# Kernel optimization log

Hardware: AMD Instinct MI355X
Metric: run time of the kernel (lower is better)

Reference implementation:

```python
import jax, jax.numpy as jnp
import numpy as np

N, D, NH, NC, B, NL = 400, 256, 4, 2, 64, 2
HD = D // NH


def _ln(x, g, b, eps=1e-5):
    mu = x.mean(-1, keepdims=True)
    var = ((x - mu) ** 2).mean(-1, keepdims=True)
    return (x - mu) * jax.lax.rsqrt(var + eps) * g + b


def _mha(q, kv, wqkv, bqkv, wo, bo):
    # torch nn.MultiheadAttention (batch_first), eval mode
    wq, wk, wv = jnp.split(wqkv, 3, axis=0)
    bq, bk, bv = jnp.split(bqkv, 3, axis=0)
    Bsz, Sq, _ = q.shape
    Sk = kv.shape[1]
    qh = (q @ wq.T + bq).reshape(Bsz, Sq, NH, HD).transpose(0, 2, 1, 3)
    kh = (kv @ wk.T + bk).reshape(Bsz, Sk, NH, HD).transpose(0, 2, 1, 3)
    vh = (kv @ wv.T + bv).reshape(Bsz, Sk, NH, HD).transpose(0, 2, 1, 3)
    scores = jnp.einsum('bhqd,bhkd->bhqk', qh, kh) / jnp.sqrt(jnp.float32(HD))
    attn = jax.nn.softmax(scores, axis=-1)
    o = jnp.einsum('bhqk,bhkd->bhqd', attn, vh)
    o = o.transpose(0, 2, 1, 3).reshape(Bsz, Sq, D)
    return o @ wo.T + bo


def setup_inputs() -> dict:
    key = jax.random.key(0)
    ks = iter(jax.random.split(key, 64))
    w = lambda *s: (jax.random.normal(next(ks), s, dtype=jnp.float32) * 0.02)
    inp = {
        'fc_matrix': jax.random.uniform(next(ks), (B, N, N), dtype=jnp.float32),
        'sc_matrix': jax.random.uniform(next(ks), (B, N, N), dtype=jnp.float32),
        'proj_w': w(D, N), 'proj_b': jnp.zeros((D,), jnp.float32),
        'enc_qkv_w': w(NL, 3 * D, D), 'enc_qkv_b': jnp.zeros((NL, 3 * D), jnp.float32),
        'enc_out_w': w(NL, D, D), 'enc_out_b': jnp.zeros((NL, D), jnp.float32),
        'enc_lin1_w': w(NL, 4 * D, D), 'enc_lin1_b': jnp.zeros((NL, 4 * D), jnp.float32),
        'enc_lin2_w': w(NL, D, 4 * D), 'enc_lin2_b': jnp.zeros((NL, D), jnp.float32),
        'enc_n1_g': jnp.ones((NL, D), jnp.float32), 'enc_n1_b': jnp.zeros((NL, D), jnp.float32),
        'enc_n2_g': jnp.ones((NL, D), jnp.float32), 'enc_n2_b': jnp.zeros((NL, D), jnp.float32),
        'gcn_w1': w(D, N), 'gcn_b1': jnp.zeros((D,), jnp.float32),
        'gcn_w2': w(D, D), 'gcn_b2': jnp.zeros((D,), jnp.float32),
        'ca1_qkv_w': w(3 * D, D), 'ca1_qkv_b': jnp.zeros((3 * D,), jnp.float32),
        'ca1_out_w': w(D, D), 'ca1_out_b': jnp.zeros((D,), jnp.float32),
        'ca1_n_g': jnp.ones((D,), jnp.float32), 'ca1_n_b': jnp.zeros((D,), jnp.float32),
        'ca2_qkv_w': w(3 * D, D), 'ca2_qkv_b': jnp.zeros((3 * D,), jnp.float32),
        'ca2_out_w': w(D, D), 'ca2_out_b': jnp.zeros((D,), jnp.float32),
        'ca2_n_g': jnp.ones((D,), jnp.float32), 'ca2_n_b': jnp.zeros((D,), jnp.float32),
        'cls_w1': w(128, N * D), 'cls_b1': jnp.zeros((128,), jnp.float32),
        'cls_w2': w(NC, 128), 'cls_b2': jnp.zeros((NC,), jnp.float32),
    }
    return inp


def reference(fc_matrix, sc_matrix, proj_w, proj_b,
              enc_qkv_w, enc_qkv_b, enc_out_w, enc_out_b,
              enc_lin1_w, enc_lin1_b, enc_lin2_w, enc_lin2_b,
              enc_n1_g, enc_n1_b, enc_n2_g, enc_n2_b,
              gcn_w1, gcn_b1, gcn_w2, gcn_b2,
              ca1_qkv_w, ca1_qkv_b, ca1_out_w, ca1_out_b, ca1_n_g, ca1_n_b,
              ca2_qkv_w, ca2_qkv_b, ca2_out_w, ca2_out_b, ca2_n_g, ca2_n_b,
              cls_w1, cls_b1, cls_w2, cls_b2):
    # ---- FC branch: input proj + 2 post-norm transformer encoder layers ----
    h = fc_matrix @ proj_w.T + proj_b  # [B,N,D]
    for l in range(NL):
        a = _mha(h, h, enc_qkv_w[l], enc_qkv_b[l], enc_out_w[l], enc_out_b[l])
        h = _ln(h + a, enc_n1_g[l], enc_n1_b[l])
        ff = jax.nn.relu(h @ enc_lin1_w[l].T + enc_lin1_b[l]) @ enc_lin2_w[l].T + enc_lin2_b[l]
        h = _ln(h + ff, enc_n2_g[l], enc_n2_b[l])
    Z_F = h

    # ---- SC branch: dense-equivalent of per-sample nonzero()+GCNConv ----
    # all entries of sc are nonzero -> edge set == dense adjacency (self-loops present,
    # so add_remaining_self_loops is a no-op). deg = in-degree (column sums of weights).
    deg = sc_matrix.sum(axis=-2)  # [B,N]
    dinv = jnp.where(deg > 0, jax.lax.rsqrt(deg), 0.0)
    An = dinv[:, :, None] * sc_matrix * dinv[:, None, :]  # An[b,i,j] = dinv_i * w_ij * dinv_j
    h1 = jnp.einsum('bij,bid->bjd', An, sc_matrix @ gcn_w1.T) + gcn_b1  # aggregate src->dst
    h1 = jax.nn.relu(h1)
    Z_S = jnp.einsum('bij,bid->bjd', An, h1 @ gcn_w2.T) + gcn_b2  # [B,N,D]

    # ---- Cross attention (eval: dropout = identity) ----
    Z_F_cross = _ln(Z_F + _mha(Z_F, Z_S, ca1_qkv_w, ca1_qkv_b, ca1_out_w, ca1_out_b), ca1_n_g, ca1_n_b)
    Z_S_cross = _ln(Z_S + _mha(Z_S, Z_F, ca2_qkv_w, ca2_qkv_b, ca2_out_w, ca2_out_b), ca2_n_g, ca2_n_b)

    Z_joint = (Z_F_cross + Z_S_cross) * 0.5
    flat = Z_joint.reshape(Z_joint.shape[0], -1)  # [B, N*D]
    logits = jax.nn.relu(flat @ cls_w1.T + cls_b1) @ cls_w2.T + cls_b2
    return logits
```

## Files before the change

### kernel.cpp

```cpp
#include <hip/hip_runtime.h>
#include <math.h>

#define NB   64
#define NN   400
#define DD   256
#define NHH  4
#define HDD  64
#define MR   25600

typedef __attribute__((ext_vector_type(8))) short bf16x8;
typedef __attribute__((ext_vector_type(4))) float f32x4;

__device__ __forceinline__ short f2bf(float x) {
    union { float f; unsigned u; } v; v.f = x;
    return (short)((v.u + 0x7FFFu + ((v.u >> 16) & 1u)) >> 16);
}
__device__ __forceinline__ float bf2f(short s) {
    union { unsigned u; float f; } v; v.u = ((unsigned)(unsigned short)s) << 16;
    return v.f;
}
__device__ __forceinline__ void gl_lds16(const void* g, void* l) {
    __builtin_amdgcn_global_load_lds(
        (const __attribute__((address_space(1))) unsigned*)g,
        (__attribute__((address_space(3))) unsigned*)l, 16, 0, 0);
}
__device__ __forceinline__ void wait_vmcnt(int n) {
    switch (n) {
    case 0: asm volatile("s_waitcnt vmcnt(0)" ::: "memory"); break;
    case 1: asm volatile("s_waitcnt vmcnt(1)" ::: "memory"); break;
    case 2: asm volatile("s_waitcnt vmcnt(2)" ::: "memory"); break;
    case 3: asm volatile("s_waitcnt vmcnt(3)" ::: "memory"); break;
    case 4: asm volatile("s_waitcnt vmcnt(4)" ::: "memory"); break;
    default: asm volatile("s_waitcnt vmcnt(5)" ::: "memory"); break;
    }
}
__device__ __forceinline__ void barrier_raw() {
    __builtin_amdgcn_sched_barrier(0);
    __builtin_amdgcn_s_barrier();
    __builtin_amdgcn_sched_barrier(0);
}


__global__ __launch_bounds__(256) void gemm_p8(
    const short* __restrict__ A, int arows, long long sA,
    const short* __restrict__ B, int brows, long long sB,
    const float* __restrict__ bias,
    short* __restrict__ C, int crows, int crz, long long sCe,
    int M, int N, int Npad, int K, int relu)
{
    __shared__ short lds[24576];
    const int tid = threadIdx.x;
    const int z = blockIdx.z;
    const int m0 = blockIdx.x * 128, n0 = blockIdx.y * 128;
    const short* Ab = A + (size_t)z * sA;
    const short* Bb = B + (size_t)z * sB;

    const int w = tid >> 6, lane = tid & 63;
    const int quad = lane >> 4, l15 = lane & 15;
    const int wm = w & 1, wn = w >> 1;

    f32x4 acc[4][4] = {};

    const int KT = K >> 5;

    auto STAGE = [&](int buf, int kt) {
        const int gp0 = kt << 2;
        short* Al = lds + buf * 8192;
        short* Bl = Al + 4096;
#pragma unroll
        for (int i = 0; i < 4; ++i) {
            int c = i * 4 + w;
            int p = (c >> 1) & 3, hh = c & 1;
            if (c < 8)
                gl_lds16(Ab + ((size_t)(gp0 + p) * arows + m0 + hh * 64 + lane) * 8,
                         &Al[(p * 128 + hh * 64) * 8]);
            else
                gl_lds16(Bb + ((size_t)(gp0 + p) * brows + n0 + hh * 64 + lane) * 8,
                         &Bl[(p * 128 + hh * 64) * 8]);
        }
    };

    STAGE(0, 0);
    STAGE(1, 1);
    for (int kt = 0; kt < KT; ++kt) {
        wait_vmcnt(kt + 1 < KT ? 4 : 0);
        barrier_raw();
        if (kt + 2 < KT) STAGE((kt + 2) % 3, kt + 2);
        const short* Al = lds + (kt % 3) * 8192;
        const short* Bl = Al + 4096;
        bf16x8 af[4], bfr[4];
#pragma unroll
        for (int mi = 0; mi < 4; ++mi)
            af[mi] = *reinterpret_cast<const bf16x8*>(
                &Al[(quad * 128 + wm * 64 + mi * 16 + l15) * 8]);
#pragma unroll
        for (int ni = 0; ni < 4; ++ni)
            bfr[ni] = *reinterpret_cast<const bf16x8*>(
                &Bl[(quad * 128 + wn * 64 + ni * 16 + l15) * 8]);
#pragma unroll
        for (int mi = 0; mi < 4; ++mi)
#pragma unroll
            for (int ni = 0; ni < 4; ++ni)
                acc[mi][ni] = __builtin_amdgcn_mfma_f32_16x16x32_bf16(af[mi], bfr[ni], acc[mi][ni], 0, 0, 0);
    }
    __syncthreads();

#pragma unroll
    for (int mi = 0; mi < 4; ++mi) {
#pragma unroll
        for (int r = 0; r < 4; ++r) {
            int row = wm * 64 + mi * 16 + quad * 4 + r;
#pragma unroll
            for (int ni = 0; ni < 4; ++ni) {
                int col = wn * 64 + ni * 16 + l15;
                int gcol = n0 + col;
                float v = 0.0f;
                if (gcol < N) {
                    v = acc[mi][ni][r];
                    if (bias) v += bias[gcol];
                    if (relu) v = fmaxf(v, 0.0f);
                }
                lds[row * 136 + col] = f2bf(v);
            }
        }
    }
    __syncthreads();
    short* Cbz = C + (size_t)z * sCe;
    const long long zr = (long long)z * crz;
#pragma unroll
    for (int t = 0; t < 8; ++t) {
        int c = t * 256 + tid;
        int row = c & 127, p16 = c >> 7;
        int grow = m0 + row;
        int gcol0 = n0 + p16 * 8;
        if (grow < M && gcol0 < Npad) {
            bf16x8 v = *reinterpret_cast<const bf16x8*>(&lds[row * 136 + p16 * 8]);
            *reinterpret_cast<bf16x8*>(
                &Cbz[((size_t)(gcol0 >> 3) * crows + zr + grow) * 8]) = v;
        }
    }
}

__global__ __launch_bounds__(256) void gemm_ln(
    const short* __restrict__ A,
    const short* __restrict__ B, int brows,
    const float* __restrict__ bias,
    const short* __restrict__ resid,
    const float* __restrict__ g, const float* __restrict__ bb,
    short* __restrict__ out, int K)
{
    __shared__ short lds[30720];
    __shared__ float gs[256], bs[256], bi_s[256];
    __shared__ float red[2][4][64];
    const int tid = threadIdx.x;
    const int m0 = blockIdx.x * 64;
    const int w = tid >> 6, lane = tid & 63;
    const int quad = lane >> 4, l15 = lane & 15;
    gs[tid] = g[tid]; bs[tid] = bb[tid]; bi_s[tid] = bias[tid];

    f32x4 acc[4][4] = {};
    const int KT = K >> 5;

    auto STAGE = [&](int buf, int kt) {
        const int gp0 = kt << 2;
        short* Al = lds + buf * 10240;
        short* Bl = Al + 2048;
#pragma unroll
        for (int i = 0; i < 5; ++i) {
            int c = i * 4 + w;
            if (c < 4) {
                gl_lds16(A + ((size_t)(gp0 + c) * MR + m0 + lane) * 8, &Al[(c * 64) * 8]);
            } else {
                int cb = c - 4, p = cb >> 2, cq = cb & 3;
                gl_lds16(B + ((size_t)(gp0 + p) * brows + cq * 64 + lane) * 8,
                         &Bl[(p * 256 + cq * 64) * 8]);
            }
        }
    };

    STAGE(0, 0);
    STAGE(1, 1);
    for (int kt = 0; kt < KT; ++kt) {
        wait_vmcnt(kt + 1 < KT ? 5 : 0);
        barrier_raw();
        if (kt + 2 < KT) STAGE((kt + 2) % 3, kt + 2);
        const short* Al = lds + (kt % 3) * 10240;
        const short* Bl = Al + 2048;
        bf16x8 af[4], bfr[4];
#pragma unroll
        for (int mi = 0; mi < 4; ++mi)
            af[mi] = *reinterpret_cast<const bf16x8*>(
                &Al[(quad * 64 + mi * 16 + l15) * 8]);
#pragma unroll
        for (int ni = 0; ni < 4; ++ni)
            bfr[ni] = *reinterpret_cast<const bf16x8*>(
                &Bl[(quad * 256 + w * 64 + ni * 16 + l15) * 8]);
#pragma unroll
        for (int mi = 0; mi < 4; ++mi)
#pragma unroll
            for (int ni = 0; ni < 4; ++ni)
                acc[mi][ni] = __builtin_amdgcn_mfma_f32_16x16x32_bf16(af[mi], bfr[ni], acc[mi][ni], 0, 0, 0);
    }
    __syncthreads();

    short* rowt = lds;
#pragma unroll
    for (int mi = 0; mi < 4; ++mi)
#pragma unroll
        for (int ni = 0; ni < 4; ++ni) {
            int col = w * 64 + ni * 16 + l15;
#pragma unroll
            for (int r = 0; r < 4; ++r) {
                int row = mi * 16 + quad * 4 + r;
                rowt[row * 264 + w * 66 + ni * 16 + l15] = f2bf(acc[mi][ni][r] + bi_s[col]);
            }
        }
    __syncthreads();

    const int row = tid >> 2, part = tid & 3;
    const int grow = m0 + row;
    float vv[8][8];
    float sum = 0.0f, sq = 0.0f;
#pragma unroll
    for (int i = 0; i < 8; ++i) {
        int plane = part * 8 + i;
        bf16x8 rv = *reinterpret_cast<const bf16x8*>(resid + ((size_t)plane * MR + grow) * 8);
        bf16x8 tv = *reinterpret_cast<const bf16x8*>(&rowt[row * 264 + part * 66 + i * 8]);
#pragma unroll
        for (int e = 0; e < 8; ++e) {
            float v = bf2f(tv[e]) + bf2f(rv[e]);
            vv[i][e] = v; sum += v; sq += v * v;
        }
    }
    red[0][part][row] = sum; red[1][part][row] = sq;
    __syncthreads();
    sum = red[0][0][row] + red[0][1][row] + red[0][2][row] + red[0][3][row];
    sq  = red[1][0][row] + red[1][1][row] + red[1][2][row] + red[1][3][row];
    float mu = sum * (1.0f / 256.0f);
    float var = sq * (1.0f / 256.0f) - mu * mu;
    float rstd = 1.0f / sqrtf(fmaxf(var, 0.0f) + 1e-5f);
#pragma unroll
    for (int i = 0; i < 8; ++i) {
        int plane = part * 8 + i;
        bf16x8 o;
#pragma unroll
        for (int e = 0; e < 8; ++e)
            o[e] = f2bf((vv[i][e] - mu) * rstd * gs[plane * 8 + e] + bs[plane * 8 + e]);
        *reinterpret_cast<bf16x8*>(out + ((size_t)plane * MR + grow) * 8) = o;
    }
}

__global__ __launch_bounds__(256) void vtrans(
    const short* __restrict__ qkv, short* __restrict__ vT)
{
    __shared__ short tile[64][66];
    const int id = blockIdx.x;
    const int xcd = id & 7, rem = id >> 3;
    const int bh_hi = rem / 7, c = rem - bh_hi * 7;
    const int bh_i = bh_hi * 8 + xcd;
    const int h = bh_i & 3, b = bh_i >> 2;
    const int tid = threadIdx.x;
    const size_t bh = (size_t)bh_i;
    for (int t = tid; t < 512; t += 256) {
        int pp = t >> 6, l = t & 63;
        int j = c * 64 + l;
        bf16x8 v;
        if (j < NN)
            v = *reinterpret_cast<const bf16x8*>(
                qkv + (((size_t)(64 + 8 * h + pp)) * MR + (size_t)b * NN + j) * 8);
        else { for (int e = 0; e < 8; ++e) v[e] = 0; }
#pragma unroll
        for (int e = 0; e < 8; ++e) tile[l][pp * 8 + e] = v[e];
    }
    __syncthreads();
    for (int t = tid; t < 512; t += 256) {
        int kq = t >> 6, d = t & 63;
        int kp = c * 8 + kq;
        bf16x8 o;
#pragma unroll
        for (int e = 0; e < 8; ++e) o[e] = tile[kq * 8 + e][d];
        *reinterpret_cast<bf16x8*>(vT + ((bh * 56 + kp) * 64 + d) * 8) = o;
    }
}

__global__ __launch_bounds__(256, 3) void attn_p8(
    const short* __restrict__ qkv, const short* __restrict__ vT,
    short* __restrict__ Out)
{
    __shared__ short PS[26624];
    const int id = blockIdx.x;
    const int xcd = id & 7, rem = id >> 3;
    const int bh_hi = rem / 7, qt = rem - bh_hi * 7;
    const int bh_i = bh_hi * 8 + xcd;
    const int h = bh_i & 3, b = bh_i >> 2;
    const int tid = threadIdx.x;
    const int w = tid >> 6, lane = tid & 63;
    const int quad = lane >> 4, l15 = lane & 15;
    const size_t rowb = (size_t)b * NN;

    for (int j = w; j < 8; j += 4)
        gl_lds16(qkv + (((size_t)(8 * h + j)) * MR + rowb + qt * 64 + lane) * 8, &PS[j * 512]);
    __syncthreads();

    bf16x8 aq0 = *reinterpret_cast<const bf16x8*>(&PS[(quad * 64 + w * 16 + l15) * 8]);
    bf16x8 aq1 = *reinterpret_cast<const bf16x8*>(&PS[((4 + quad) * 64 + w * 16 + l15) * 8]);

    const short* Kb0 = qkv + ((size_t)(32 + 8 * h + quad) * MR + rowb + l15) * 8;
    const short* Kb1 = qkv + ((size_t)(36 + 8 * h + quad) * MR + rowb + l15) * 8;

    f32x4 sacc[25];
#pragma unroll
    for (int nt = 0; nt < 25; ++nt) { sacc[nt][0] = 0; sacc[nt][1] = 0; sacc[nt][2] = 0; sacc[nt][3] = 0; }
#pragma unroll
    for (int nt = 0; nt < 25; ++nt) {
        bf16x8 b0 = *reinterpret_cast<const bf16x8*>(Kb0 + nt * 128);
        bf16x8 b1 = *reinterpret_cast<const bf16x8*>(Kb1 + nt * 128);
        sacc[nt] = __builtin_amdgcn_mfma_f32_16x16x32_bf16(aq0, b0, sacc[nt], 0, 0, 0);
        sacc[nt] = __builtin_amdgcn_mfma_f32_16x16x32_bf16(aq1, b1, sacc[nt], 0, 0, 0);
    }

    float mx[4] = {-3e38f, -3e38f, -3e38f, -3e38f}, sm[4] = {0, 0, 0, 0};
#pragma unroll
    for (int nt = 0; nt < 25; ++nt)
#pragma unroll
        for (int r = 0; r < 4; ++r) mx[r] = fmaxf(mx[r], sacc[nt][r]);
#pragma unroll
    for (int r = 0; r < 4; ++r) {
        mx[r] = fmaxf(mx[r], __shfl_xor(mx[r], 1));
        mx[r] = fmaxf(mx[r], __shfl_xor(mx[r], 2));
        mx[r] = fmaxf(mx[r], __shfl_xor(mx[r], 4));
        mx[r] = fmaxf(mx[r], __shfl_xor(mx[r], 8));
    }
#pragma unroll
    for (int nt = 0; nt < 25; ++nt)
#pragma unroll
        for (int r = 0; r < 4; ++r) {
            float e = __expf((sacc[nt][r] - mx[r]) * 0.125f);
            sacc[nt][r] = e;
            sm[r] += e;
        }
#pragma unroll
    for (int r = 0; r < 4; ++r) {
        sm[r] += __shfl_xor(sm[r], 1);
        sm[r] += __shfl_xor(sm[r], 2);
        sm[r] += __shfl_xor(sm[r], 4);
        sm[r] += __shfl_xor(sm[r], 8);
    }
    __syncthreads();

#pragma unroll
    for (int nt = 0; nt < 25; ++nt)
#pragma unroll
        for (int r = 0; r < 4; ++r) {
            int colk = nt * 16 + l15;
            PS[((colk >> 3) * 64 + w * 16 + quad * 4 + r) * 8 + (colk & 7)] = f2bf(sacc[nt][r]);
        }
    for (int idx = tid; idx < 1024; idx += 256) PS[25600 + idx] = 0;

    f32x4 oacc[4];
#pragma unroll
    for (int dt = 0; dt < 4; ++dt) { oacc[dt][0] = 0; oacc[dt][1] = 0; oacc[dt][2] = 0; oacc[dt][3] = 0; }
    __syncthreads();

    const short* Vb = vT + (((size_t)bh_i * 56 + quad) * 64 + l15) * 8;
#pragma unroll
    for (int kt = 0; kt < 13; ++kt) {
        bf16x8 pa = *reinterpret_cast<const bf16x8*>(
            &PS[((kt * 4 + quad) * 64 + w * 16 + l15) * 8]);
#pragma unroll
        for (int dt = 0; dt < 4; ++dt) {
            bf16x8 vb = *reinterpret_cast<const bf16x8*>(Vb + kt * 2048 + dt * 128);
            oacc[dt] = __builtin_amdgcn_mfma_f32_16x16x32_bf16(pa, vb, oacc[dt], 0, 0, 0);
        }
    }
#pragma unroll
    for (int r = 0; r < 4; ++r) {
        int row = qt * 64 + w * 16 + quad * 4 + r;
        if (row >= NN) continue;
        float inv = 1.0f / sm[r];
#pragma unroll
        for (int dt = 0; dt < 4; ++dt) {
            int col = dt * 16 + l15;
            Out[(((size_t)(8 * h + (col >> 3))) * MR + rowb + row) * 8 + (col & 7)] =
                f2bf(oacc[dt][r] * inv);
        }
    }
}

__global__ void conv_p8(const float* __restrict__ src, short* __restrict__ dst,
                        int R, int K, int Kp, int PR)
{
    const int G = Kp >> 3;
    int idx = blockIdx.x * 256 + threadIdx.x;
    if (idx >= R * G) return;
    int r = idx / G, g = idx - r * G;
    int k0 = g << 3;
    bf16x8 o;
    if (k0 + 8 <= K) {
        const float4 v0 = *reinterpret_cast<const float4*>(src + (size_t)r * K + k0);
        const float4 v1 = *reinterpret_cast<const float4*>(src + (size_t)r * K + k0 + 4);
        o[0] = f2bf(v0.x); o[1] = f2bf(v0.y); o[2] = f2bf(v0.z); o[3] = f2bf(v0.w);
        o[4] = f2bf(v1.x); o[5] = f2bf(v1.y); o[6] = f2bf(v1.z); o[7] = f2bf(v1.w);
    } else {
#pragma unroll
        for (int e = 0; e < 8; ++e) {
            int k = k0 + e;
            o[e] = (k < K) ? f2bf(src[(size_t)r * K + k]) : (short)0;
        }
    }
    *reinterpret_cast<bf16x8*>(dst + ((size_t)g * PR + r) * 8) = o;
}

__global__ __launch_bounds__(256) void w1_p8(
    const float* __restrict__ W1, short* __restrict__ Wp)
{
    __shared__ float tile[128][129];
    const int k0 = blockIdx.x * 128;
    const int tid = threadIdx.x;
    for (int t = 0; t < 16; ++t) {
        int idx = t * 256 + tid;
        int r = idx >> 5, k4 = idx & 31;
        float4 v = *(const float4*)(W1 + (size_t)r * 102400 + k0 + k4 * 4);
        tile[r][k4 * 4 + 0] = v.x; tile[r][k4 * 4 + 1] = v.y;
        tile[r][k4 * 4 + 2] = v.z; tile[r][k4 * 4 + 3] = v.w;
    }
    __syncthreads();
    for (int t = 0; t < 8; ++t) {
        int idx = t * 256 + tid;
        int pidx = idx >> 7, r = idx & 127;
        bf16x8 o;
#pragma unroll
        for (int e = 0; e < 8; ++e) o[e] = f2bf(tile[r][pidx * 8 + e]);
        *reinterpret_cast<bf16x8*>(Wp + (((size_t)(k0 >> 3) + pidx) * 128 + r) * 8) = o;
    }
}

__global__ void colsum_dinv(const float* __restrict__ sc, float* __restrict__ dinv)
{
    int b = blockIdx.y;
    int j = blockIdx.x * 256 + threadIdx.x;
    if (j >= NN) return;
    const float* p = sc + (size_t)b * NN * NN + j;
    float s = 0.0f;
    for (int i = 0; i < NN; ++i) s += p[(size_t)i * NN];
    dinv[b * NN + j] = (s > 0.0f) ? 1.0f / sqrtf(s) : 0.0f;
}

__global__ __launch_bounds__(256) void sc_prep(
    const float* __restrict__ sc, const float* __restrict__ dinv,
    short* __restrict__ scb, short* __restrict__ anT)
{
    __shared__ float tile[64][65];
    const int b = blockIdx.z;
    const int i0 = blockIdx.y * 64, j0 = blockIdx.x * 64;
    const int tid = threadIdx.x;
    const float* sb = sc + (size_t)b * NN * NN;
    short* scbb = scb + (size_t)b * 56 * 512 * 8;
    short* anTb = anT + (size_t)b * 56 * 512 * 8;
    for (int e = tid; e < 4096; e += 256) {
        int r = e >> 6, c = e & 63;
        int i = i0 + r, j = j0 + c;
        tile[r][c] = (i < NN && j < NN) ? sb[(size_t)i * NN + j] : 0.0f;
    }
    __syncthreads();
    for (int e = tid; e < 4096; e += 256) {
        int r = e >> 6, c = e & 63;
        int i = i0 + r, j = j0 + c;
        scbb[((size_t)(j >> 3) * 512 + i) * 8 + (j & 7)] = f2bf(tile[r][c]);
        float v = 0.0f;
        if (i < NN && j < NN) v = tile[r][c] * dinv[b * NN + i] * dinv[b * NN + j];
        anTb[((size_t)(i >> 3) * 512 + j) * 8 + (i & 7)] = f2bf(v);
    }
}

__global__ __launch_bounds__(256) void cls_gemm(
    const short* __restrict__ C1, const short* __restrict__ C2,
    const short* __restrict__ Wp, float* __restrict__ partial)
{
    __shared__ short Al[32 * 64 * 8];
    __shared__ short Wl[8 * 128 * 8];
    const int j = blockIdx.x;
    const int tid = threadIdx.x;
    const int w = tid >> 6, lane = tid & 63;
    const int quad = lane >> 4, l15 = lane & 15;

    for (int s = 0; s < 8; ++s) {
        int idx = s * 256 + tid;
        int p = idx >> 6, b = idx & 63;
        size_t ad = ((size_t)p * MR + (size_t)b * NN + j) * 8;
        bf16x8 a = *reinterpret_cast<const bf16x8*>(C1 + ad);
        bf16x8 c = *reinterpret_cast<const bf16x8*>(C2 + ad);
        bf16x8 o;
#pragma unroll
        for (int e = 0; e < 8; ++e) o[e] = f2bf(0.5f * (bf2f(a[e]) + bf2f(c[e])));
        *reinterpret_cast<bf16x8*>(&Al[(p * 64 + b) * 8]) = o;
    }

    f32x4 acc[4][2] = {};
    const size_t wp0 = (size_t)j * 32;
    for (int s = 0; s < 4; ++s) {
#pragma unroll
        for (int pp = 0; pp < 2; ++pp) {
            int p = w + pp * 4;
            gl_lds16(Wp + ((wp0 + s * 8 + p) * 128 + lane) * 8,      &Wl[(p * 128) * 8]);
            gl_lds16(Wp + ((wp0 + s * 8 + p) * 128 + 64 + lane) * 8, &Wl[(p * 128 + 64) * 8]);
        }
        __syncthreads();
#pragma unroll
        for (int kb = 0; kb < 2; ++kb) {
            bf16x8 af[4], bfr[2];
#pragma unroll
            for (int mi = 0; mi < 4; ++mi)
                af[mi] = *reinterpret_cast<const bf16x8*>(
                    &Al[((s * 8 + kb * 4 + quad) * 64 + mi * 16 + l15) * 8]);
#pragma unroll
            for (int ni = 0; ni < 2; ++ni)
                bfr[ni] = *reinterpret_cast<const bf16x8*>(
                    &Wl[((kb * 4 + quad) * 128 + w * 32 + ni * 16 + l15) * 8]);
#pragma unroll
            for (int mi = 0; mi < 4; ++mi)
#pragma unroll
                for (int ni = 0; ni < 2; ++ni)
                    acc[mi][ni] = __builtin_amdgcn_mfma_f32_16x16x32_bf16(af[mi], bfr[ni], acc[mi][ni], 0, 0, 0);
        }
        __syncthreads();
    }
    float* pj = partial + (size_t)j * 8192;
#pragma unroll
    for (int mi = 0; mi < 4; ++mi)
#pragma unroll
        for (int r = 0; r < 4; ++r) {
            int row = mi * 16 + quad * 4 + r;
#pragma unroll
            for (int ni = 0; ni < 2; ++ni)
                pj[row * 128 + w * 32 + ni * 16 + l15] = acc[mi][ni][r];
        }
}

__global__ void cls_reduce(const float* __restrict__ partial, float* __restrict__ clsh)
{
    int o = blockIdx.x * 256 + threadIdx.x;
    float s = 0.0f;
    for (int kb = 0; kb < 400; ++kb) s += partial[(size_t)kb * 8192 + o];
    clsh[o] = s;
}

__global__ void logits_final(
    const float* __restrict__ clsh, const float* __restrict__ b1,
    const float* __restrict__ w2, const float* __restrict__ b2,
    float* __restrict__ out)
{
    __shared__ float t[128];
    int b = blockIdx.x;
    int tid = threadIdx.x;
    t[tid] = fmaxf(clsh[b * 128 + tid] + b1[tid], 0.0f);
    __syncthreads();
    if (tid < 2) {
        float s = b2[tid];
        for (int o = 0; o < 128; ++o) s += t[o] * w2[tid * 128 + o];
        out[b * 2 + tid] = s;
    }
}

extern "C" void kernel_launch(void* const* d_in, const int* in_sizes, int n_in,
                              void* d_out, int out_size, void* d_ws, size_t ws_size,
                              hipStream_t stream)
{
    const float* fc        = (const float*)d_in[0];
    const float* sc        = (const float*)d_in[1];
    const float* proj_w    = (const float*)d_in[2];
    const float* proj_b    = (const float*)d_in[3];
    const float* enc_qkv_w = (const float*)d_in[4];
    const float* enc_qkv_b = (const float*)d_in[5];
    const float* enc_out_w = (const float*)d_in[6];
    const float* enc_out_b = (const float*)d_in[7];
    const float* enc_l1_w  = (const float*)d_in[8];
    const float* enc_l1_b  = (const float*)d_in[9];
    const float* enc_l2_w  = (const float*)d_in[10];
    const float* enc_l2_b  = (const float*)d_in[11];
    const float* enc_n1_g  = (const float*)d_in[12];
    const float* enc_n1_b  = (const float*)d_in[13];
    const float* enc_n2_g  = (const float*)d_in[14];
    const float* enc_n2_b  = (const float*)d_in[15];
    const float* gcn_w1    = (const float*)d_in[16];
    const float* gcn_b1    = (const float*)d_in[17];
    const float* gcn_w2    = (const float*)d_in[18];
    const float* gcn_b2    = (const float*)d_in[19];
    const float* ca1_qkv_w = (const float*)d_in[20];
    const float* ca1_qkv_b = (const float*)d_in[21];
    const float* ca1_out_w = (const float*)d_in[22];
    const float* ca1_out_b = (const float*)d_in[23];
    const float* ca1_n_g   = (const float*)d_in[24];
    const float* ca1_n_b   = (const float*)d_in[25];
    const float* ca2_qkv_w = (const float*)d_in[26];
    const float* ca2_qkv_b = (const float*)d_in[27];
    const float* ca2_out_w = (const float*)d_in[28];
    const float* ca2_out_b = (const float*)d_in[29];
    const float* ca2_n_g   = (const float*)d_in[30];
    const float* ca2_n_b   = (const float*)d_in[31];
    const float* cls_w1    = (const float*)d_in[32];
    const float* cls_b1    = (const float*)d_in[33];
    const float* cls_w2    = (const float*)d_in[34];
    const float* cls_b2    = (const float*)d_in[35];

    char* wsb = (char*)d_ws;
    size_t off = 0;
    auto alloc = [&](size_t bytes) { char* r = wsb + off; off += (bytes + 255) & ~(size_t)255; return r; };
    short* bufBig = (short*)alloc((size_t)MR * 1024 * 2);
    short* fcb    = (short*)alloc((size_t)56 * MR * 8 * 2);
    short* anT    = (short*)alloc((size_t)NB * 56 * 512 * 8 * 2);
    short* bufH   = (short*)alloc((size_t)32 * MR * 8 * 2);
    short* bufA   = (short*)alloc((size_t)32 * MR * 8 * 2);
    short* bufC   = (short*)alloc((size_t)32 * MR * 8 * 2);
    short* bufZS  = (short*)alloc((size_t)32 * MR * 8 * 2);
    short* vT     = (short*)alloc((size_t)NB * NHH * 56 * 64 * 8 * 2);
    short* w1b    = (short*)alloc((size_t)12800 * 128 * 8 * 2);
    short* projwb = (short*)alloc((size_t)56 * 256 * 8 * 2);
    short* qkvwb  = (short*)alloc((size_t)32 * 1536 * 8 * 2);
    short* outwb  = (short*)alloc((size_t)32 * 512 * 8 * 2);
    short* l1wb   = (short*)alloc((size_t)32 * 2048 * 8 * 2);
    short* l2wb   = (short*)alloc((size_t)128 * 512 * 8 * 2);
    short* gw1b   = (short*)alloc((size_t)56 * 256 * 8 * 2);
    short* gw2b   = (short*)alloc((size_t)32 * 256 * 8 * 2);
    short* c1qb   = (short*)alloc((size_t)32 * 768 * 8 * 2);
    short* c1ob   = (short*)alloc((size_t)32 * 256 * 8 * 2);
    short* c2qb   = (short*)alloc((size_t)32 * 768 * 8 * 2);
    short* c2ob   = (short*)alloc((size_t)32 * 256 * 8 * 2);
    float* dinv   = (float*)alloc((size_t)MR * 4);
    float* clsh   = (float*)alloc((size_t)NB * 128 * 4);
    short* scb = bufBig;
    short* XT1 = bufBig + (size_t)64 * 56 * 512 * 8;
    short* h1  = bufBig;
    short* XT2 = XT1;
    float* partial = (float*)fcb;

    dim3 blk(256);
    auto cgrid = [](long long n) { return dim3((unsigned)((n + 255) / 256)); };

    conv_p8<<<cgrid((long long)MR * 56), blk, 0, stream>>>(fc, fcb, MR, 400, 448, MR);
    conv_p8<<<cgrid(256 * 56), blk, 0, stream>>>(proj_w, projwb, 256, 400, 448, 256);
    conv_p8<<<cgrid(1536 * 32), blk, 0, stream>>>(enc_qkv_w, qkvwb, 1536, 256, 256, 1536);
    conv_p8<<<cgrid(512 * 32), blk, 0, stream>>>(enc_out_w, outwb, 512, 256, 256, 512);
    conv_p8<<<cgrid(2048 * 32), blk, 0, stream>>>(enc_l1_w, l1wb, 2048, 256, 256, 2048);
    conv_p8<<<cgrid(512 * 128), blk, 0, stream>>>(enc_l2_w, l2wb, 512, 1024, 1024, 512);
    conv_p8<<<cgrid(256 * 56), blk, 0, stream>>>(gcn_w1, gw1b, 256, 400, 448, 256);
    conv_p8<<<cgrid(256 * 32), blk, 0, stream>>>(gcn_w2, gw2b, 256, 256, 256, 256);
    conv_p8<<<cgrid(768 * 32), blk, 0, stream>>>(ca1_qkv_w, c1qb, 768, 256, 256, 768);
    conv_p8<<<cgrid(256 * 32), blk, 0, stream>>>(ca1_out_w, c1ob, 256, 256, 256, 256);
    conv_p8<<<cgrid(768 * 32), blk, 0, stream>>>(ca2_qkv_w, c2qb, 768, 256, 256, 768);
    conv_p8<<<cgrid(256 * 32), blk, 0, stream>>>(ca2_out_w, c2ob, 256, 256, 256, 256);
    w1_p8<<<800, blk, 0, stream>>>(cls_w1, w1b);

    gemm_p8<<<dim3(200, 2, 1), blk, 0, stream>>>(
        fcb, MR, 0, projwb, 256, 0, proj_b, bufH, MR, 0, 0, MR, 256, 256, 448, 0);
    for (int l = 0; l < 2; ++l) {
        gemm_p8<<<dim3(200, 6, 1), blk, 0, stream>>>(
            bufH, MR, 0, qkvwb + (size_t)l * 768 * 8, 1536, 0, enc_qkv_b + l * 768,
            bufBig, MR, 0, 0, MR, 768, 768, 256, 0);
        vtrans<<<dim3(1792), blk, 0, stream>>>(bufBig, vT);
        attn_p8<<<dim3(1792), blk, 0, stream>>>(bufBig, vT, bufA);
        gemm_ln<<<400, blk, 0, stream>>>(
            bufA, outwb + (size_t)l * 256 * 8, 512, enc_out_b + l * 256,
            bufH, enc_n1_g + l * DD, enc_n1_b + l * DD, bufH, 256);
        gemm_p8<<<dim3(200, 8, 1), blk, 0, stream>>>(
            bufH, MR, 0, l1wb + (size_t)l * 1024 * 8, 2048, 0, enc_l1_b + l * 1024,
            bufBig, MR, 0, 0, MR, 1024, 1024, 256, 1);
        gemm_ln<<<400, blk, 0, stream>>>(
            bufBig, l2wb + (size_t)l * 256 * 8, 512, enc_l2_b + l * 256,
            bufH, enc_n2_g + l * DD, enc_n2_b + l * DD, bufH, 1024);
    }

    colsum_dinv<<<dim3(2, NB), blk, 0, stream>>>(sc, dinv);
    sc_prep<<<dim3(7, 7, NB), blk, 0, stream>>>(sc, dinv, scb, anT);
    gemm_p8<<<dim3(2, 4, NB), blk, 0, stream>>>(
        gw1b, 256, 0, scb, 512, 56LL * 512 * 8, nullptr,
        XT1, 256, 0, 56LL * 256 * 8, 256, 400, 448, 448, 0);
    gemm_p8<<<dim3(4, 2, NB), blk, 0, stream>>>(
        anT, 512, 56LL * 512 * 8, XT1, 256, 56LL * 256 * 8, gcn_b1,
        h1, 512, 0, 32LL * 512 * 8, 400, 256, 256, 448, 1);
    gemm_p8<<<dim3(2, 4, NB), blk, 0, stream>>>(
        gw2b, 256, 0, h1, 512, 32LL * 512 * 8, nullptr,
        XT2, 256, 0, 56LL * 256 * 8, 256, 400, 448, 256, 0);
    gemm_p8<<<dim3(4, 2, NB), blk, 0, stream>>>(
        anT, 512, 56LL * 512 * 8, XT2, 256, 56LL * 256 * 8, gcn_b2,
        bufZS, MR, 400, 0, 400, 256, 256, 448, 0);

    gemm_p8<<<dim3(200, 2, 1), blk, 0, stream>>>(
        bufH, MR, 0, c1qb, 768, 0, ca1_qkv_b, bufBig, MR, 0, 0, MR, 256, 256, 256, 0);
    gemm_p8<<<dim3(200, 4, 1), blk, 0, stream>>>(
        bufZS, MR, 0, c1qb + 256 * 8, 768, 0, ca1_qkv_b + 256,
        bufBig + (size_t)32 * MR * 8, MR, 0, 0, MR, 512, 512, 256, 0);
    vtrans<<<dim3(1792), blk, 0, stream>>>(bufBig, vT);
    attn_p8<<<dim3(1792), blk, 0, stream>>>(bufBig, vT, bufA);
    gemm_ln<<<400, blk, 0, stream>>>(
        bufA, c1ob, 256, ca1_out_b, bufH, ca1_n_g, ca1_n_b, bufC, 256);

    gemm_p8<<<dim3(200, 2, 1), blk, 0, stream>>>(
        bufZS, MR, 0, c2qb, 768, 0, ca2_qkv_b, bufBig, MR, 0, 0, MR, 256, 256, 256, 0);
    gemm_p8<<<dim3(200, 4, 1), blk, 0, stream>>>(
        bufH, MR, 0, c2qb + 256 * 8, 768, 0, ca2_qkv_b + 256,
        bufBig + (size_t)32 * MR * 8, MR, 0, 0, MR, 512, 512, 256, 0);
    vtrans<<<dim3(1792), blk, 0, stream>>>(bufBig, vT);
    attn_p8<<<dim3(1792), blk, 0, stream>>>(bufBig, vT, bufA);
    gemm_ln<<<400, blk, 0, stream>>>(
        bufA, c2ob, 256, ca2_out_b, bufZS, ca2_n_g, ca2_n_b, bufZS, 256);

    cls_gemm<<<400, blk, 0, stream>>>(bufC, bufZS, w1b, partial);
    cls_reduce<<<32, blk, 0, stream>>>(partial, clsh);
    logits_final<<<NB, 128, 0, stream>>>(clsh, cls_b1, cls_w2, cls_b2, (float*)d_out);
}
```

Measured before the change: 970.3 us.

## Enlarge GEMM tile to 256x128 with 512 threads and batch weight conversions

The bf16 MFMA GEMM now computes a 256x128 output tile per block using 8 waves, up from 128x128 with 4. Each B tile loaded into LDS is therefore reused across twice as many rows, which cuts global traffic for the weight operand. The LDS ring buffer, stage mapping, vmcnt wait count and epilogue indexing are resized to match, and all launch grids are halved along M. Separately, eleven weight float-to-bf16 conversion launches are merged into one segmented kernel to save launch overhead. The `__launch_bounds__(512, 4)` hint may cap registers tightly enough to force accumulator spills, and fewer blocks means less parallelism on the smaller GCN GEMMs.

```diff
diff --git a/kernel.cpp b/kernel.cpp
--- a/kernel.cpp
+++ b/kernel.cpp
@@ -41,23 +41,23 @@
 }
 
 
-__global__ __launch_bounds__(256) void gemm_p8(
+__global__ __launch_bounds__(512, 4) void gemm_p8(
     const short* __restrict__ A, int arows, long long sA,
     const short* __restrict__ B, int brows, long long sB,
     const float* __restrict__ bias,
     short* __restrict__ C, int crows, int crz, long long sCe,
     int M, int N, int Npad, int K, int relu)
 {
-    __shared__ short lds[24576];
+    __shared__ short lds[36864];
     const int tid = threadIdx.x;
     const int z = blockIdx.z;
-    const int m0 = blockIdx.x * 128, n0 = blockIdx.y * 128;
+    const int m0 = blockIdx.x * 256, n0 = blockIdx.y * 128;
     const short* Ab = A + (size_t)z * sA;
     const short* Bb = B + (size_t)z * sB;
 
     const int w = tid >> 6, lane = tid & 63;
     const int quad = lane >> 4, l15 = lane & 15;
-    const int wm = w & 1, wn = w >> 1;
+    const int wm = w & 3, wn = w >> 2;
 
     f32x4 acc[4][4] = {};
 
@@ -65,34 +65,36 @@
 
     auto STAGE = [&](int buf, int kt) {
         const int gp0 = kt << 2;
-        short* Al = lds + buf * 8192;
-        short* Bl = Al + 4096;
-#pragma unroll
-        for (int i = 0; i < 4; ++i) {
-            int c = i * 4 + w;
-            int p = (c >> 1) & 3, hh = c & 1;
-            if (c < 8)
+        short* Al = lds + buf * 12288;
+        short* Bl = Al + 8192;
+#pragma unroll
+        for (int i = 0; i < 3; ++i) {
+            int c = i * 8 + w;
+            if (c < 16) {
+                int p = c >> 2, hh = c & 3;
                 gl_lds16(Ab + ((size_t)(gp0 + p) * arows + m0 + hh * 64 + lane) * 8,
-                         &Al[(p * 128 + hh * 64) * 8]);
-            else
+                         &Al[(p * 256 + hh * 64) * 8]);
+            } else {
+                int cb = c - 16, p = cb >> 1, hh = cb & 1;
                 gl_lds16(Bb + ((size_t)(gp0 + p) * brows + n0 + hh * 64 + lane) * 8,
                          &Bl[(p * 128 + hh * 64) * 8]);
+            }
         }
     };
 
     STAGE(0, 0);
     STAGE(1, 1);
     for (int kt = 0; kt < KT; ++kt) {
-        wait_vmcnt(kt + 1 < KT ? 4 : 0);
+        wait_vmcnt(kt + 1 < KT ? 3 : 0);
         barrier_raw();
         if (kt + 2 < KT) STAGE((kt + 2) % 3, kt + 2);
-        const short* Al = lds + (kt % 3) * 8192;
-        const short* Bl = Al + 4096;
+        const short* Al = lds + (kt % 3) * 12288;
+        const short* Bl = Al + 8192;
         bf16x8 af[4], bfr[4];
 #pragma unroll
         for (int mi = 0; mi < 4; ++mi)
             af[mi] = *reinterpret_cast<const bf16x8*>(
-                &Al[(quad * 128 + wm * 64 + mi * 16 + l15) * 8]);
+                &Al[(quad * 256 + wm * 64 + mi * 16 + l15) * 8]);
 #pragma unroll
         for (int ni = 0; ni < 4; ++ni)
             bfr[ni] = *reinterpret_cast<const bf16x8*>(
@@ -129,8 +131,8 @@
     const long long zr = (long long)z * crz;
 #pragma unroll
     for (int t = 0; t < 8; ++t) {
-        int c = t * 256 + tid;
-        int row = c & 127, p16 = c >> 7;
+        int c = t * 512 + tid;
+        int row = c & 255, p16 = c >> 8;
         int grow = m0 + row;
         int gcol0 = n0 + p16 * 8;
         if (grow < M && gcol0 < Npad) {
@@ -409,6 +411,37 @@
         }
     }
     *reinterpret_cast<bf16x8*>(dst + ((size_t)g * PR + r) * 8) = o;
+}
+
+struct ConvSeg { const float* src; short* dst; int R, K, Kp, start; };
+struct ConvPack { ConvSeg s[11]; int total; };
+
+__global__ void conv_multi(ConvPack p)
+{
+    int idx = blockIdx.x * 256 + threadIdx.x;
+    if (idx >= p.total) return;
+    int si = 0;
+#pragma unroll
+    for (int t = 1; t < 11; ++t) if (idx >= p.s[t].start) si = t;
+    const ConvSeg sg = p.s[si];
+    int local = idx - sg.start;
+    const int G = sg.Kp >> 3;
+    int r = local / G, g = local - r * G;
+    int k0 = g << 3;
+    bf16x8 o;
+    if (k0 + 8 <= sg.K) {
+        const float4 v0 = *reinterpret_cast<const float4*>(sg.src + (size_t)r * sg.K + k0);
+        const float4 v1 = *reinterpret_cast<const float4*>(sg.src + (size_t)r * sg.K + k0 + 4);
+        o[0] = f2bf(v0.x); o[1] = f2bf(v0.y); o[2] = f2bf(v0.z); o[3] = f2bf(v0.w);
+        o[4] = f2bf(v1.x); o[5] = f2bf(v1.y); o[6] = f2bf(v1.z); o[7] = f2bf(v1.w);
+    } else {
+#pragma unroll
+        for (int e = 0; e < 8; ++e) {
+            int k = k0 + e;
+            o[e] = (k < sg.K) ? f2bf(sg.src[(size_t)r * sg.K + k]) : (short)0;
+        }
+    }
+    *reinterpret_cast<bf16x8*>(sg.dst + ((size_t)g * sg.R + r) * 8) = o;
 }
 
 __global__ __launch_bounds__(256) void w1_p8(
@@ -634,27 +667,37 @@
     short* XT2 = XT1;
     float* partial = (float*)fcb;
 
-    dim3 blk(256);
+    dim3 blk(256), blk512(512);
     auto cgrid = [](long long n) { return dim3((unsigned)((n + 255) / 256)); };
 
     conv_p8<<<cgrid((long long)MR * 56), blk, 0, stream>>>(fc, fcb, MR, 400, 448, MR);
-    conv_p8<<<cgrid(256 * 56), blk, 0, stream>>>(proj_w, projwb, 256, 400, 448, 256);
-    conv_p8<<<cgrid(1536 * 32), blk, 0, stream>>>(enc_qkv_w, qkvwb, 1536, 256, 256, 1536);
-    conv_p8<<<cgrid(512 * 32), blk, 0, stream>>>(enc_out_w, outwb, 512, 256, 256, 512);
-    conv_p8<<<cgrid(2048 * 32), blk, 0, stream>>>(enc_l1_w, l1wb, 2048, 256, 256, 2048);
-    conv_p8<<<cgrid(512 * 128), blk, 0, stream>>>(enc_l2_w, l2wb, 512, 1024, 1024, 512);
-    conv_p8<<<cgrid(256 * 56), blk, 0, stream>>>(gcn_w1, gw1b, 256, 400, 448, 256);
-    conv_p8<<<cgrid(256 * 32), blk, 0, stream>>>(gcn_w2, gw2b, 256, 256, 256, 256);
-    conv_p8<<<cgrid(768 * 32), blk, 0, stream>>>(ca1_qkv_w, c1qb, 768, 256, 256, 768);
-    conv_p8<<<cgrid(256 * 32), blk, 0, stream>>>(ca1_out_w, c1ob, 256, 256, 256, 256);
-    conv_p8<<<cgrid(768 * 32), blk, 0, stream>>>(ca2_qkv_w, c2qb, 768, 256, 256, 768);
-    conv_p8<<<cgrid(256 * 32), blk, 0, stream>>>(ca2_out_w, c2ob, 256, 256, 256, 256);
+    {
+        ConvPack pk;
+        int st = 0;
+        auto seg = [&](int i, const float* s, short* d, int R, int K, int Kp) {
+            pk.s[i].src = s; pk.s[i].dst = d; pk.s[i].R = R; pk.s[i].K = K;
+            pk.s[i].Kp = Kp; pk.s[i].start = st; st += R * (Kp >> 3);
+        };
+        seg(0,  proj_w,    projwb, 256,  400,  448);
+        seg(1,  enc_qkv_w, qkvwb,  1536, 256,  256);
+        seg(2,  enc_out_w, outwb,  512,  256,  256);
+        seg(3,  enc_l1_w,  l1wb,   2048, 256,  256);
+        seg(4,  enc_l2_w,  l2wb,   512,  1024, 1024);
+        seg(5,  gcn_w1,    gw1b,   256,  400,  448);
+        seg(6,  gcn_w2,    gw2b,   256,  256,  256);
+        seg(7,  ca1_qkv_w, c1qb,   768,  256,  256);
+        seg(8,  ca1_out_w, c1ob,   256,  256,  256);
+        seg(9,  ca2_qkv_w, c2qb,   768,  256,  256);
+        seg(10, ca2_out_w, c2ob,   256,  256,  256);
+        pk.total = st;
+        conv_multi<<<cgrid(st), blk, 0, stream>>>(pk);
+    }
     w1_p8<<<800, blk, 0, stream>>>(cls_w1, w1b);
 
-    gemm_p8<<<dim3(200, 2, 1), blk, 0, stream>>>(
+    gemm_p8<<<dim3(100, 2, 1), blk512, 0, stream>>>(
         fcb, MR, 0, projwb, 256, 0, proj_b, bufH, MR, 0, 0, MR, 256, 256, 448, 0);
     for (int l = 0; l < 2; ++l) {
-        gemm_p8<<<dim3(200, 6, 1), blk, 0, stream>>>(
+        gemm_p8<<<dim3(100, 6, 1), blk512, 0, stream>>>(
             bufH, MR, 0, qkvwb + (size_t)l * 768 * 8, 1536, 0, enc_qkv_b + l * 768,
             bufBig, MR, 0, 0, MR, 768, 768, 256, 0);
         vtrans<<<dim3(1792), blk, 0, stream>>>(bufBig, vT);
@@ -662,7 +705,7 @@
         gemm_ln<<<400, blk, 0, stream>>>(
             bufA, outwb + (size_t)l * 256 * 8, 512, enc_out_b + l * 256,
             bufH, enc_n1_g + l * DD, enc_n1_b + l * DD, bufH, 256);
-        gemm_p8<<<dim3(200, 8, 1), blk, 0, stream>>>(
+        gemm_p8<<<dim3(100, 8, 1), blk512, 0, stream>>>(
             bufH, MR, 0, l1wb + (size_t)l * 1024 * 8, 2048, 0, enc_l1_b + l * 1024,
             bufBig, MR, 0, 0, MR, 1024, 1024, 256, 1);
         gemm_ln<<<400, blk, 0, stream>>>(
@@ -672,22 +715,22 @@
 
     colsum_dinv<<<dim3(2, NB), blk, 0, stream>>>(sc, dinv);
     sc_prep<<<dim3(7, 7, NB), blk, 0, stream>>>(sc, dinv, scb, anT);
-    gemm_p8<<<dim3(2, 4, NB), blk, 0, stream>>>(
+    gemm_p8<<<dim3(1, 4, NB), blk512, 0, stream>>>(
         gw1b, 256, 0, scb, 512, 56LL * 512 * 8, nullptr,
         XT1, 256, 0, 56LL * 256 * 8, 256, 400, 448, 448, 0);
-    gemm_p8<<<dim3(4, 2, NB), blk, 0, stream>>>(
+    gemm_p8<<<dim3(2, 2, NB), blk512, 0, stream>>>(
         anT, 512, 56LL * 512 * 8, XT1, 256, 56LL * 256 * 8, gcn_b1,
         h1, 512, 0, 32LL * 512 * 8, 400, 256, 256, 448, 1);
-    gemm_p8<<<dim3(2, 4, NB), blk, 0, stream>>>(
+    gemm_p8<<<dim3(1, 4, NB), blk512, 0, stream>>>(
         gw2b, 256, 0, h1, 512, 32LL * 512 * 8, nullptr,
         XT2, 256, 0, 56LL * 256 * 8, 256, 400, 448, 256, 0);
-    gemm_p8<<<dim3(4, 2, NB), blk, 0, stream>>>(
+    gemm_p8<<<dim3(2, 2, NB), blk512, 0, stream>>>(
         anT, 512, 56LL * 512 * 8, XT2, 256, 56LL * 256 * 8, gcn_b2,
         bufZS, MR, 400, 0, 400, 256, 256, 448, 0);
 
-    gemm_p8<<<dim3(200, 2, 1), blk, 0, stream>>>(
+    gemm_p8<<<dim3(100, 2, 1), blk512, 0, stream>>>(
         bufH, MR, 0, c1qb, 768, 0, ca1_qkv_b, bufBig, MR, 0, 0, MR, 256, 256, 256, 0);
-    gemm_p8<<<dim3(200, 4, 1), blk, 0, stream>>>(
+    gemm_p8<<<dim3(100, 4, 1), blk512, 0, stream>>>(
         bufZS, MR, 0, c1qb + 256 * 8, 768, 0, ca1_qkv_b + 256,
         bufBig + (size_t)32 * MR * 8, MR, 0, 0, MR, 512, 512, 256, 0);
     vtrans<<<dim3(1792), blk, 0, stream>>>(bufBig, vT);
@@ -695,9 +738,9 @@
     gemm_ln<<<400, blk, 0, stream>>>(
         bufA, c1ob, 256, ca1_out_b, bufH, ca1_n_g, ca1_n_b, bufC, 256);
 
-    gemm_p8<<<dim3(200, 2, 1), blk, 0, stream>>>(
+    gemm_p8<<<dim3(100, 2, 1), blk512, 0, stream>>>(
         bufZS, MR, 0, c2qb, 768, 0, ca2_qkv_b, bufBig, MR, 0, 0, MR, 256, 256, 256, 0);
-    gemm_p8<<<dim3(200, 4, 1), blk, 0, stream>>>(
+    gemm_p8<<<dim3(100, 4, 1), blk512, 0, stream>>>(
         bufH, MR, 0, c2qb + 256 * 8, 768, 0, ca2_qkv_b + 256,
         bufBig + (size_t)32 * MR * 8, MR, 0, 0, MR, 512, 512, 256, 0);
     vtrans<<<dim3(1792), blk, 0, stream>>>(bufBig, vT);
```

After: 940.5 us. -3.1%, faster.
